# Kernel optimization log

Hardware: AMD Instinct MI355X
Metric: run time of the kernel (lower is better)

## Reference

```python
import jax, jax.numpy as jnp
import numpy as np

PATCH = 16

def setup_inputs() -> dict:
    key = jax.random.key(0)
    k1, k2 = jax.random.split(key)
    B, C, H, W = 256, 3, 224, 224
    x = jax.random.normal(k1, (B, C, H, W), dtype=jnp.float32)
    # Bernoulli(p=0.5) sample per patch, per batch element: shape (B, W//P, H//P)
    mask = jax.random.randint(k2, (B, W // PATCH, H // PATCH), 0, 2).astype(jnp.bool_)
    return {"x": x, "mask": mask}

def reference(x, mask):
    B, C, H, W = x.shape
    P = PATCH
    h, w = H // P, W // P
    # rearrange 'b c (h p1) (w p2) -> b w h p1 p2 c'
    patches = x.reshape(B, C, h, P, w, P).transpose(0, 4, 2, 3, 5, 1)  # (B, w, h, P, P, C)
    # conditional per-patch transpose 'p1 p2 c -> p2 p1 c' where mask is True
    rotated = jnp.swapaxes(patches, 3, 4)
    patches = jnp.where(mask[:, :, :, None, None, None], rotated, patches)
    # rearrange 'b w h p2 p1 c -> b c (h p2) (w p1)'
    out = patches.transpose(0, 5, 2, 3, 1, 4).reshape(B, C, H, W)
    return out
```

## Files before the change

### kernel.cpp

```cpp
#include <hip/hip_runtime.h>


#define NPATCH 14

typedef float f4 __attribute__((ext_vector_type(4)));

__device__ __forceinline__ float bperm(int idx, float s) {
    return __int_as_float(__builtin_amdgcn_ds_bpermute(idx, __float_as_int(s)));
}

__global__ __launch_bounds__(256) void patch_rotate_kernel(
    const float* __restrict__ x,
    const int*   __restrict__ mask,
    float*       __restrict__ out)
{
    const int tid  = threadIdx.x;
    const int lane = tid & 63;
    const int wv   = tid >> 6;
    const int w    = blockIdx.x * 4 + wv;

    const int p  = lane >> 4;
    const int a  = (lane >> 2) & 3;
    const int bb = lane & 3;
    const int lp = (lane & 48) | (bb << 2) | a;
    const int idx = lp << 2;

    #pragma unroll
    for (int uu = 0; uu < 2; ++uu) {
        const int u   = 2 * w + uu;
        const int img = u / 49;
        const int q   = u % 49;
        const int n   = 4 * q + p;
        const int hi  = n / NPATCH;
        const int wi  = n % NPATCH;
        const int b   = img / 3;

        const int row = hi * 16 + 4 * a;
        const int col = wi * 16 + 4 * bb;
        const size_t base = ((size_t)img * 224 + row) * 224 + col;

        const f4 v0 = __builtin_nontemporal_load((const f4*)(x + base));
        const f4 v1 = __builtin_nontemporal_load((const f4*)(x + base + 224));
        const f4 v2 = __builtin_nontemporal_load((const f4*)(x + base + 448));
        const f4 v3 = __builtin_nontemporal_load((const f4*)(x + base + 672));

        const int m = mask[(b * NPATCH + wi) * NPATCH + hi];

        f4 B0, B1, B2, B3;
        B0.x = bperm(idx, v0.x); B0.y = bperm(idx, v0.y);
        B0.z = bperm(idx, v0.z); B0.w = bperm(idx, v0.w);
        B1.x = bperm(idx, v1.x); B1.y = bperm(idx, v1.y);
        B1.z = bperm(idx, v1.z); B1.w = bperm(idx, v1.w);
        B2.x = bperm(idx, v2.x); B2.y = bperm(idx, v2.y);
        B2.z = bperm(idx, v2.z); B2.w = bperm(idx, v2.w);
        B3.x = bperm(idx, v3.x); B3.y = bperm(idx, v3.y);
        B3.z = bperm(idx, v3.z); B3.w = bperm(idx, v3.w);

        f4 r0 = v0, r1 = v1, r2 = v2, r3 = v3;
        if (m) {
            r0.x = B0.x; r0.y = B1.x; r0.z = B2.x; r0.w = B3.x;
            r1.x = B0.y; r1.y = B1.y; r1.z = B2.y; r1.w = B3.y;
            r2.x = B0.z; r2.y = B1.z; r2.z = B2.z; r2.w = B3.z;
            r3.x = B0.w; r3.y = B1.w; r3.z = B2.w; r3.w = B3.w;
        }

        __builtin_nontemporal_store(r0, (f4*)(out + base));
        __builtin_nontemporal_store(r1, (f4*)(out + base + 224));
        __builtin_nontemporal_store(r2, (f4*)(out + base + 448));
        __builtin_nontemporal_store(r3, (f4*)(out + base + 672));
    }
}

extern "C" void kernel_launch(void* const* d_in, const int* in_sizes, int n_in,
                              void* d_out, int out_size, void* d_ws, size_t ws_size,
                              hipStream_t stream) {
    const float* x    = (const float*)d_in[0];
    const int*   mask = (const int*)d_in[1];
    float*       out  = (float*)d_out;

    patch_rotate_kernel<<<4704, 256, 0, stream>>>(x, mask, out);
}
```

Measured before the change: 251.6 us.

## Software-pipeline 8 units per wave with prefetch and fewer blocks

Each wave now handles 8 patch-units instead of 2, loading the next unit's data and mask before permuting and storing the current one, and the grid shrinks to a quarter. Nontemporal loads and stores become ordinary ones, and launch bounds ask for 8 blocks per CU. The aim is more loads in flight per wave and less per-block launch overhead. In exchange it holds more registers and gives fewer waves across the device, and dropping the nontemporal hints may change cache behaviour.

```diff
diff --git a/kernel.cpp b/kernel.cpp
--- a/kernel.cpp
+++ b/kernel.cpp
@@ -9,7 +9,66 @@
     return __int_as_float(__builtin_amdgcn_ds_bpermute(idx, __float_as_int(s)));
 }
 
-__global__ __launch_bounds__(256) void patch_rotate_kernel(
+struct Unit {
+    size_t base;
+    int    m;
+    f4     v0, v1, v2, v3;
+};
+
+__device__ __forceinline__ void load_unit(const float* __restrict__ x,
+                                          const int*   __restrict__ mask,
+                                          int u, int p, int a, int bb,
+                                          Unit& U)
+{
+    const int img = u / 49;
+    const int q   = u - img * 49;
+    const int n   = 4 * q + p;
+    const int hi  = n / NPATCH;
+    const int wi  = n - hi * NPATCH;
+    const int b   = img / 3;
+
+    const int row = hi * 16 + 4 * a;
+    const int col = wi * 16 + 4 * bb;
+    U.base = ((size_t)img * 224 + row) * 224 + col;
+
+    U.m = mask[(b * NPATCH + wi) * NPATCH + hi];
+
+    U.v0 = *(const f4*)(x + U.base);
+    U.v1 = *(const f4*)(x + U.base + 224);
+    U.v2 = *(const f4*)(x + U.base + 448);
+    U.v3 = *(const f4*)(x + U.base + 672);
+}
+
+__device__ __forceinline__ void proc_store(float* __restrict__ out,
+                                           int idx, const Unit& U)
+{
+    const f4 v0 = U.v0, v1 = U.v1, v2 = U.v2, v3 = U.v3;
+
+    f4 B0, B1, B2, B3;
+    B0.x = bperm(idx, v0.x); B0.y = bperm(idx, v0.y);
+    B0.z = bperm(idx, v0.z); B0.w = bperm(idx, v0.w);
+    B1.x = bperm(idx, v1.x); B1.y = bperm(idx, v1.y);
+    B1.z = bperm(idx, v1.z); B1.w = bperm(idx, v1.w);
+    B2.x = bperm(idx, v2.x); B2.y = bperm(idx, v2.y);
+    B2.z = bperm(idx, v2.z); B2.w = bperm(idx, v2.w);
+    B3.x = bperm(idx, v3.x); B3.y = bperm(idx, v3.y);
+    B3.z = bperm(idx, v3.z); B3.w = bperm(idx, v3.w);
+
+    f4 r0 = v0, r1 = v1, r2 = v2, r3 = v3;
+    if (U.m) {
+        r0.x = B0.x; r0.y = B1.x; r0.z = B2.x; r0.w = B3.x;
+        r1.x = B0.y; r1.y = B1.y; r1.z = B2.y; r1.w = B3.y;
+        r2.x = B0.z; r2.y = B1.z; r2.z = B2.z; r2.w = B3.z;
+        r3.x = B0.w; r3.y = B1.w; r3.z = B2.w; r3.w = B3.w;
+    }
+
+    *(f4*)(out + U.base)       = r0;
+    *(f4*)(out + U.base + 224) = r1;
+    *(f4*)(out + U.base + 448) = r2;
+    *(f4*)(out + U.base + 672) = r3;
+}
+
+__global__ __launch_bounds__(256, 8) void patch_rotate_kernel(
     const float* __restrict__ x,
     const int*   __restrict__ mask,
     float*       __restrict__ out)
@@ -17,57 +76,22 @@
     const int tid  = threadIdx.x;
     const int lane = tid & 63;
     const int wv   = tid >> 6;
-    const int w    = blockIdx.x * 4 + wv;
+    const int wave = blockIdx.x * 4 + wv;
+    const int u0   = wave * 8;
 
     const int p  = lane >> 4;
     const int a  = (lane >> 2) & 3;
     const int bb = lane & 3;
-    const int lp = (lane & 48) | (bb << 2) | a;
-    const int idx = lp << 2;
+    const int idx = ((lane & 48) | (bb << 2) | a) << 2;
+
+    Unit cur, nxt;
+    load_unit(x, mask, u0, p, a, bb, cur);
 
     #pragma unroll
-    for (int uu = 0; uu < 2; ++uu) {
-        const int u   = 2 * w + uu;
-        const int img = u / 49;
-        const int q   = u % 49;
-        const int n   = 4 * q + p;
-        const int hi  = n / NPATCH;
-        const int wi  = n % NPATCH;
-        const int b   = img / 3;
-
-        const int row = hi * 16 + 4 * a;
-        const int col = wi * 16 + 4 * bb;
-        const size_t base = ((size_t)img * 224 + row) * 224 + col;
-
-        const f4 v0 = __builtin_nontemporal_load((const f4*)(x + base));
-        const f4 v1 = __builtin_nontemporal_load((const f4*)(x + base + 224));
-        const f4 v2 = __builtin_nontemporal_load((const f4*)(x + base + 448));
-        const f4 v3 = __builtin_nontemporal_load((const f4*)(x + base + 672));
-
-        const int m = mask[(b * NPATCH + wi) * NPATCH + hi];
-
-        f4 B0, B1, B2, B3;
-        B0.x = bperm(idx, v0.x); B0.y = bperm(idx, v0.y);
-        B0.z = bperm(idx, v0.z); B0.w = bperm(idx, v0.w);
-        B1.x = bperm(idx, v1.x); B1.y = bperm(idx, v1.y);
-        B1.z = bperm(idx, v1.z); B1.w = bperm(idx, v1.w);
-        B2.x = bperm(idx, v2.x); B2.y = bperm(idx, v2.y);
-        B2.z = bperm(idx, v2.z); B2.w = bperm(idx, v2.w);
-        B3.x = bperm(idx, v3.x); B3.y = bperm(idx, v3.y);
-        B3.z = bperm(idx, v3.z); B3.w = bperm(idx, v3.w);
-
-        f4 r0 = v0, r1 = v1, r2 = v2, r3 = v3;
-        if (m) {
-            r0.x = B0.x; r0.y = B1.x; r0.z = B2.x; r0.w = B3.x;
-            r1.x = B0.y; r1.y = B1.y; r1.z = B2.y; r1.w = B3.y;
-            r2.x = B0.z; r2.y = B1.z; r2.z = B2.z; r2.w = B3.z;
-            r3.x = B0.w; r3.y = B1.w; r3.z = B2.w; r3.w = B3.w;
-        }
-
-        __builtin_nontemporal_store(r0, (f4*)(out + base));
-        __builtin_nontemporal_store(r1, (f4*)(out + base + 224));
-        __builtin_nontemporal_store(r2, (f4*)(out + base + 448));
-        __builtin_nontemporal_store(r3, (f4*)(out + base + 672));
+    for (int j = 0; j < 8; ++j) {
+        if (j < 7) load_unit(x, mask, u0 + j + 1, p, a, bb, nxt);
+        proc_store(out, idx, cur);
+        if (j < 7) cur = nxt;
     }
 }
 
@@ -78,5 +102,5 @@
     const int*   mask = (const int*)d_in[1];
     float*       out  = (float*)d_out;
 
-    patch_rotate_kernel<<<4704, 256, 0, stream>>>(x, mask, out);
+    patch_rotate_kernel<<<1176, 256, 0, stream>>>(x, mask, out);
 }
```

After: 268.2 us. 1.07x slower.
